# Optimization experiments

Hardware: AMD Instinct MI355X
Metric: run time of the kernel (lower is better)

Reference implementation:

```python
import jax, jax.numpy as jnp
import numpy as np

INPUT_SIZE = 64
HIDDEN = 512
NUM_CLASSES = 10


def setup_inputs() -> dict:
    key = jax.random.key(0)
    ks = jax.random.split(key, 9)
    B, T = 1024, 256
    bound_lstm = 1.0 / np.sqrt(HIDDEN)
    bound_lin = 1.0 / np.sqrt(HIDDEN)
    x = jax.random.normal(ks[0], (B, T * INPUT_SIZE), dtype=jnp.float32)
    h0 = jax.random.normal(ks[1], (B, HIDDEN), dtype=jnp.float32)
    c0 = jax.random.normal(ks[2], (B, HIDDEN), dtype=jnp.float32)
    W_ih = jax.random.uniform(ks[3], (4 * HIDDEN, INPUT_SIZE), jnp.float32, -bound_lstm, bound_lstm)
    W_hh = jax.random.uniform(ks[4], (4 * HIDDEN, HIDDEN), jnp.float32, -bound_lstm, bound_lstm)
    b_ih = jax.random.uniform(ks[5], (4 * HIDDEN,), jnp.float32, -bound_lstm, bound_lstm)
    b_hh = jax.random.uniform(ks[6], (4 * HIDDEN,), jnp.float32, -bound_lstm, bound_lstm)
    W_lin = jax.random.uniform(ks[7], (NUM_CLASSES, HIDDEN), jnp.float32, -bound_lin, bound_lin)
    b_lin = jax.random.uniform(ks[8], (NUM_CLASSES,), jnp.float32, -bound_lin, bound_lin)
    return {"x": x, "h0": h0, "c0": c0, "W_ih": W_ih, "W_hh": W_hh,
            "b_ih": b_ih, "b_hh": b_hh, "W_lin": W_lin, "b_lin": b_lin}


def _lstm_forward(x, h0, c0, W_ih, W_hh, b_ih, b_hh, W_lin, b_lin):
    B = x.shape[0]
    T = x.shape[1] // INPUT_SIZE
    # [B, T*in] -> [T, B, in]; torch.split along dim 1 gives contiguous chunks
    xs = x.reshape(B, T, INPUT_SIZE).transpose(1, 0, 2)
    # precompute input projections for all steps: [T, B, 4H]
    gates_x = jnp.einsum('tbi,gi->tbg', xs, W_ih) + b_ih + b_hh

    def step(carry, gx):
        h, c = carry
        gates = gx + h @ W_hh.T  # [B, 4H], torch gate order i,f,g,o
        i, f, g, o = jnp.split(gates, 4, axis=-1)
        i = jax.nn.sigmoid(i)
        f = jax.nn.sigmoid(f)
        g = jnp.tanh(g)
        o = jax.nn.sigmoid(o)
        c_new = f * c + i * g
        h_new = o * jnp.tanh(c_new)
        return (h_new, c_new), None

    (hT, cT), _ = jax.lax.scan(step, (h0, c0), gates_x)
    preds = hT @ W_lin.T + b_lin  # [B, 10]
    return preds


def reference(x, h0, c0, W_ih, W_hh, b_ih, b_hh, W_lin, b_lin):
    return _lstm_forward(x, h0, c0, W_ih, W_hh, b_ih, b_hh, W_lin, b_lin)
```

## Files before the change

kernel.cpp:

```cpp
#include <hip/hip_runtime.h>
#include <hip/hip_bf16.h>


#define TST   256
#define BATCH 1024
#define HID   512
#define INSZ  64
#define NCLS  10
#define LDSTR 584

typedef _Float16 f16x8  __attribute__((ext_vector_type(8)));
typedef float    f32x16 __attribute__((ext_vector_type(16)));
typedef unsigned long long u64;

__device__ __forceinline__ float tanh_f(float x) {
    return 2.0f / (1.0f + __expf(-2.0f * x)) - 1.0f;
}

__device__ __forceinline__ f16x8 cvt8(float4 a, float4 b) {
    f16x8 o;
    o[0] = (_Float16)a.x; o[1] = (_Float16)a.y; o[2] = (_Float16)a.z; o[3] = (_Float16)a.w;
    o[4] = (_Float16)b.x; o[5] = (_Float16)b.y; o[6] = (_Float16)b.z; o[7] = (_Float16)b.w;
    return o;
}

__device__ __forceinline__ u64 cvt4_u64(float4 a) {
    _Float16 h[4] = {(_Float16)a.x, (_Float16)a.y, (_Float16)a.z, (_Float16)a.w};
    u64 r;
    __builtin_memcpy(&r, h, 8);
    return r;
}

template <int CTRL>
__device__ __forceinline__ float dpp_f(float v) {
    return __builtin_bit_cast(float,
        __builtin_amdgcn_mov_dpp(__builtin_bit_cast(int, v), CTRL, 0xF, 0xF, true));
}
template <int CTRL>
__device__ __forceinline__ unsigned dpp_u(unsigned v) {
    return (unsigned)__builtin_amdgcn_mov_dpp((int)v, CTRL, 0xF, 0xF, true);
}

__global__ __launch_bounds__(256, 1) void lstm_persist(
    const float* __restrict__ x,   const float* __restrict__ h0,
    const float* __restrict__ c0,  const float* __restrict__ Wih,
    const float* __restrict__ Whh, const float* __restrict__ bih,
    const float* __restrict__ bhh, _Float16* __restrict__ hb,
    unsigned* __restrict__ bar)
{
    __shared__ __align__(16) _Float16 As[32][LDSTR];

    const int tid   = threadIdx.x;
    const int lane  = tid & 63;
    const int w     = tid >> 6;
    const int l31   = lane & 31;
    const int khalf = (lane >> 5) * 8;
    const int g  = (int)(blockIdx.x >> 3);
    const int jb = (int)(blockIdx.x & 7);
    const int m0 = g * 32;
    const int j0 = jb * 64;
    unsigned* cnt = bar + g * 64;

    const int gate = l31 & 3;
    int jcol[2], nrow[2];
    #pragma unroll
    for (int nt = 0; nt < 2; ++nt) {
        int np = w * 64 + nt * 32 + l31;
        jcol[nt] = j0 + (np >> 2);
        nrow[nt] = gate * HID + jcol[nt];
    }

    f16x8 bfr[2][36];
    #pragma unroll
    for (int nt = 0; nt < 2; ++nt)
        #pragma unroll
        for (int kt = 0; kt < 36; ++kt) {
            const int k0 = kt * 16 + khalf;
            const float* p = (kt < 32) ? (Whh + (size_t)nrow[nt] * HID + k0)
                                       : (Wih + (size_t)nrow[nt] * INSZ + (k0 - HID));
            float4 f0 = ((const float4*)p)[0];
            float4 f1 = ((const float4*)p)[1];
            bfr[nt][kt] = cvt8(f0, f1);
        }
    float bsv[2];
    bsv[0] = bih[nrow[0]] + bhh[nrow[0]];
    bsv[1] = bih[nrow[1]] + bhh[nrow[1]];
    const float s   = (gate == 2) ? 2.0f : 1.0f;
    const int rowhi = (lane >> 5) * 4;

    float cr[2][16];
    #pragma unroll
    for (int nt = 0; nt < 2; ++nt)
        #pragma unroll
        for (int r = 0; r < 16; ++r) {
            int row = (r & 3) + 8 * (r >> 2) + rowhi;
            cr[nt][r] = c0[(size_t)(m0 + row) * HID + jcol[nt]];
        }

    const int rr = tid >> 3;
    const int q  = tid & 7;

    for (int t = 0; t < TST; ++t) {
        const _Float16* rb = hb + (size_t)((t + 2) % 3) * (BATCH * HID);
        _Float16*       wb = hb + (size_t)(t % 3) * (BATCH * HID);

        float4 x0, x1;
        {
            const float* xp = x + (size_t)(m0 + rr) * (TST * INSZ) + t * INSZ + q * 8;
            x0 = ((const float4*)xp)[0];
            x1 = ((const float4*)xp)[1];
        }
        if (t == 0) {
            u64 hv[16];
            #pragma unroll
            for (int u = 0; u < 16; ++u) {
                float4 f = *(const float4*)(h0 + (size_t)(m0 + rr) * HID + q * 4 + u * 32);
                hv[u] = cvt4_u64(f);
            }
            #pragma unroll
            for (int u = 0; u < 16; ++u)
                *(u64*)&As[rr][q * 4 + u * 32] = hv[u];
        } else {
            const u64* rbq = (const u64*)(rb + (size_t)(m0 + rr) * HID);
            u64 hv[16];
            #pragma unroll
            for (int u = 0; u < 16; ++u)
                hv[u] = __hip_atomic_load(&rbq[q + u * 8],
                                          __ATOMIC_RELAXED, __HIP_MEMORY_SCOPE_AGENT);
            #pragma unroll
            for (int u = 0; u < 16; ++u)
                *(u64*)&As[rr][q * 4 + u * 32] = hv[u];
        }
        *(f16x8*)&As[rr][512 + q * 8] = cvt8(x0, x1);
        __syncthreads();

        f32x16 acc[2];
        #pragma unroll
        for (int i = 0; i < 16; ++i) { acc[0][i] = 0.0f; acc[1][i] = 0.0f; }
        #pragma unroll
        for (int kt = 0; kt < 36; ++kt) {
            f16x8 af = *(const f16x8*)&As[l31][kt * 16 + khalf];
            acc[0] = __builtin_amdgcn_mfma_f32_32x32x16_f16(af, bfr[0][kt], acc[0], 0, 0, 0);
            acc[1] = __builtin_amdgcn_mfma_f32_32x32x16_f16(af, bfr[1][kt], acc[1], 0, 0, 0);
        }

        #pragma unroll
        for (int nt = 0; nt < 2; ++nt) {
            #pragma unroll
            for (int r = 0; r < 16; ++r) {
                float v = acc[nt][r] + bsv[nt];
                float e = __expf(-s * v);
                float act = s / (1.0f + e) - (s - 1.0f);
                float fu = dpp_f<0xB1>(act);
                float gu = dpp_f<0x4E>(act);
                float ou = dpp_f<0x1B>(act);
                float cn = fu * cr[nt][r] + act * gu;
                cr[nt][r] = cn;
                float hn = ou * tanh_f(cn);
                unsigned hu = (unsigned)__builtin_bit_cast(unsigned short, (_Float16)hn);
                unsigned pk = hu | (dpp_u<0x104>(hu) << 16);
                u64 v4 = (u64)pk | ((u64)dpp_u<0x108>(pk) << 32);
                if ((l31 & 15) == 0) {
                    int row = (r & 3) + 8 * (r >> 2) + rowhi;
                    __hip_atomic_store((u64*)&wb[(size_t)(m0 + row) * HID + jcol[nt]],
                                       v4, __ATOMIC_RELAXED, __HIP_MEMORY_SCOPE_AGENT);
                }
            }
        }

        __syncthreads();
        if (tid == 0) {
            __hip_atomic_fetch_add(cnt, 1u, __ATOMIC_RELAXED, __HIP_MEMORY_SCOPE_AGENT);
            const unsigned target = 8u * (unsigned)(t + 1);
            while (__hip_atomic_load(cnt, __ATOMIC_RELAXED, __HIP_MEMORY_SCOPE_AGENT) < target)
                __builtin_amdgcn_s_sleep(1);
        }
        __syncthreads();
    }
}

__global__ __launch_bounds__(256) void final_kernel(
    const _Float16* __restrict__ h, const float* __restrict__ Wl,
    const float* __restrict__ bl, float* __restrict__ out)
{
    int i = blockIdx.x * 256 + threadIdx.x;
    if (i >= BATCH * NCLS) return;
    int b = i / NCLS, c = i - b * NCLS;
    const f16x8* hp = (const f16x8*)(h + (size_t)b * HID);
    const float4* wp = (const float4*)(Wl + (size_t)c * HID);
    float sacc = bl[c];
    #pragma unroll 4
    for (int k8 = 0; k8 < HID / 8; ++k8) {
        f16x8 hv = hp[k8];
        float4 w0 = wp[2 * k8], w1 = wp[2 * k8 + 1];
        sacc += (float)hv[0] * w0.x + (float)hv[1] * w0.y +
                (float)hv[2] * w0.z + (float)hv[3] * w0.w +
                (float)hv[4] * w1.x + (float)hv[5] * w1.y +
                (float)hv[6] * w1.z + (float)hv[7] * w1.w;
    }
    out[i] = sacc;
}

extern "C" void kernel_launch(void* const* d_in, const int* in_sizes, int n_in,
                              void* d_out, int out_size, void* d_ws, size_t ws_size,
                              hipStream_t stream)
{
    const float* x    = (const float*)d_in[0];
    const float* h0   = (const float*)d_in[1];
    const float* c0   = (const float*)d_in[2];
    const float* Wih  = (const float*)d_in[3];
    const float* Whh  = (const float*)d_in[4];
    const float* bih  = (const float*)d_in[5];
    const float* bhh  = (const float*)d_in[6];
    const float* Wlin = (const float*)d_in[7];
    const float* blin = (const float*)d_in[8];
    float* out = (float*)d_out;

    unsigned* bar = (unsigned*)d_ws;
    _Float16* hb  = (_Float16*)((char*)d_ws + 8192);

    hipMemsetAsync(d_ws, 0, 8192, stream);

    lstm_persist<<<256, 256, 0, stream>>>(x, h0, c0, Wih, Whh, bih, bhh, hb, bar);

    final_kernel<<<(BATCH * NCLS + 255) / 256, 256, 0, stream>>>(hb, Wlin, blin, out);
}
```

Baseline: 1.881 ms.

## Replace group counter barrier with per-block step flags polled before loading h

```diff
diff --git a/kernel.cpp b/kernel.cpp
--- a/kernel.cpp
+++ b/kernel.cpp
@@ -24,13 +24,6 @@
     return o;
 }
 
-__device__ __forceinline__ u64 cvt4_u64(float4 a) {
-    _Float16 h[4] = {(_Float16)a.x, (_Float16)a.y, (_Float16)a.z, (_Float16)a.w};
-    u64 r;
-    __builtin_memcpy(&r, h, 8);
-    return r;
-}
-
 template <int CTRL>
 __device__ __forceinline__ float dpp_f(float v) {
     return __builtin_bit_cast(float,
@@ -46,7 +39,7 @@
     const float* __restrict__ c0,  const float* __restrict__ Wih,
     const float* __restrict__ Whh, const float* __restrict__ bih,
     const float* __restrict__ bhh, _Float16* __restrict__ hb,
-    unsigned* __restrict__ bar)
+    unsigned* __restrict__ done)
 {
     __shared__ __align__(16) _Float16 As[32][LDSTR];
 
@@ -59,7 +52,7 @@
     const int jb = (int)(blockIdx.x & 7);
     const int m0 = g * 32;
     const int j0 = jb * 64;
-    unsigned* cnt = bar + g * 64;
+    unsigned* gflags = done + g * 16;
 
     const int gate = l31 & 3;
     int jcol[2], nrow[2];
@@ -97,8 +90,9 @@
             cr[nt][r] = c0[(size_t)(m0 + row) * HID + jcol[nt]];
         }
 
-    const int rr = tid >> 3;
-    const int q  = tid & 7;
+    const int rr8 = tid >> 3;
+    const int q8  = tid & 7;
+    const int myp = tid & 7;
 
     for (int t = 0; t < TST; ++t) {
         const _Float16* rb = hb + (size_t)((t + 2) % 3) * (BATCH * HID);
@@ -106,37 +100,47 @@
 
         float4 x0, x1;
         {
-            const float* xp = x + (size_t)(m0 + rr) * (TST * INSZ) + t * INSZ + q * 8;
+            const float* xp = x + (size_t)(m0 + rr8) * (TST * INSZ) + t * INSZ + q8 * 8;
             x0 = ((const float4*)xp)[0];
             x1 = ((const float4*)xp)[1];
         }
+
         if (t == 0) {
+            #pragma unroll
+            for (int p = 0; p < 8; ++p) {
+                const float* hp = h0 + (size_t)(m0 + rr8) * HID + p * 64 + q8 * 8;
+                float4 f0 = ((const float4*)hp)[0];
+                float4 f1 = ((const float4*)hp)[1];
+                *(f16x8*)&As[rr8][p * 64 + q8 * 8] = cvt8(f0, f1);
+            }
+        } else {
+            while (1) {
+                unsigned fl = __hip_atomic_load(&gflags[myp],
+                                                __ATOMIC_RELAXED, __HIP_MEMORY_SCOPE_AGENT);
+                if (!__any((int)fl < t)) break;
+                __builtin_amdgcn_s_sleep(1);
+            }
+            const u64* rbq = (const u64*)(rb + (size_t)(m0 + rr8) * HID);
             u64 hv[16];
             #pragma unroll
-            for (int u = 0; u < 16; ++u) {
-                float4 f = *(const float4*)(h0 + (size_t)(m0 + rr) * HID + q * 4 + u * 32);
-                hv[u] = cvt4_u64(f);
-            }
-            #pragma unroll
-            for (int u = 0; u < 16; ++u)
-                *(u64*)&As[rr][q * 4 + u * 32] = hv[u];
-        } else {
-            const u64* rbq = (const u64*)(rb + (size_t)(m0 + rr) * HID);
-            u64 hv[16];
-            #pragma unroll
-            for (int u = 0; u < 16; ++u)
-                hv[u] = __hip_atomic_load(&rbq[q + u * 8],
-                                          __ATOMIC_RELAXED, __HIP_MEMORY_SCOPE_AGENT);
-            #pragma unroll
-            for (int u = 0; u < 16; ++u)
-                *(u64*)&As[rr][q * 4 + u * 32] = hv[u];
-        }
-        *(f16x8*)&As[rr][512 + q * 8] = cvt8(x0, x1);
+            for (int p = 0; p < 8; ++p) {
+                hv[2 * p]     = __hip_atomic_load(&rbq[p * 16 + q8 * 2],
+                                   __ATOMIC_RELAXED, __HIP_MEMORY_SCOPE_AGENT);
+                hv[2 * p + 1] = __hip_atomic_load(&rbq[p * 16 + q8 * 2 + 1],
+                                   __ATOMIC_RELAXED, __HIP_MEMORY_SCOPE_AGENT);
+            }
+            #pragma unroll
+            for (int p = 0; p < 8; ++p) {
+                *(u64*)&As[rr8][p * 64 + q8 * 8]     = hv[2 * p];
+                *(u64*)&As[rr8][p * 64 + q8 * 8 + 4] = hv[2 * p + 1];
+            }
+        }
+        *(f16x8*)&As[rr8][512 + q8 * 8] = cvt8(x0, x1);
         __syncthreads();
 
         f32x16 acc[2];
         #pragma unroll
-        for (int i = 0; i < 16; ++i) { acc[0][i] = 0.0f; acc[1][i] = 0.0f; }
+        for (int i = 0; i < 16; ++i) { acc[0][i] = bsv[0]; acc[1][i] = bsv[1]; }
         #pragma unroll
         for (int kt = 0; kt < 36; ++kt) {
             f16x8 af = *(const f16x8*)&As[l31][kt * 16 + khalf];
@@ -148,7 +152,7 @@
         for (int nt = 0; nt < 2; ++nt) {
             #pragma unroll
             for (int r = 0; r < 16; ++r) {
-                float v = acc[nt][r] + bsv[nt];
+                float v = acc[nt][r];
                 float e = __expf(-s * v);
                 float act = s / (1.0f + e) - (s - 1.0f);
                 float fu = dpp_f<0xB1>(act);
@@ -169,13 +173,9 @@
         }
 
         __syncthreads();
-        if (tid == 0) {
-            __hip_atomic_fetch_add(cnt, 1u, __ATOMIC_RELAXED, __HIP_MEMORY_SCOPE_AGENT);
-            const unsigned target = 8u * (unsigned)(t + 1);
-            while (__hip_atomic_load(cnt, __ATOMIC_RELAXED, __HIP_MEMORY_SCOPE_AGENT) < target)
-                __builtin_amdgcn_s_sleep(1);
-        }
-        __syncthreads();
+        if (tid == 0)
+            __hip_atomic_store(&gflags[jb], (unsigned)(t + 1),
+                               __ATOMIC_RELEASE, __HIP_MEMORY_SCOPE_AGENT);
     }
 }
 
@@ -216,12 +216,12 @@
     const float* blin = (const float*)d_in[8];
     float* out = (float*)d_out;
 
-    unsigned* bar = (unsigned*)d_ws;
-    _Float16* hb  = (_Float16*)((char*)d_ws + 8192);
+    unsigned* done = (unsigned*)d_ws;
+    _Float16* hb   = (_Float16*)((char*)d_ws + 8192);
 
     hipMemsetAsync(d_ws, 0, 8192, stream);
 
-    lstm_persist<<<256, 256, 0, stream>>>(x, h0, c0, Wih, Whh, bih, bhh, hb, bar);
+    lstm_persist<<<256, 256, 0, stream>>>(x, h0, c0, Wih, Whh, bih, bhh, hb, done);
 
     final_kernel<<<(BATCH * NCLS + 255) / 256, 256, 0, stream>>>(hb, Wlin, blin, out);
 }
```

After: 3.037 ms. +61.4%, slower.
